# Optimization experiments

Measured on AMD Instinct MI355X. Metric: run time of the kernel, lower is better.

## Reference

```python
import jax, jax.numpy as jnp
import numpy as np

NUM_ITER = 3
SLOT_DIM = 16
INPUT_DIM = 256
HIDDEN_DIM = 128
EPS = 1e-8
LN_EPS = 1e-5  # torch LayerNorm default


def _layernorm(x, w, b):
    mu = jnp.mean(x, axis=-1, keepdims=True)
    var = jnp.mean((x - mu) ** 2, axis=-1, keepdims=True)
    return (x - mu) * jax.lax.rsqrt(var + LN_EPS) * w + b


def setup_inputs() -> dict:
    key = jax.random.key(0)
    ks = jax.random.split(key, 12)
    B, N, K = 32, 4096, 8
    D, S, H = INPUT_DIM, SLOT_DIM, HIDDEN_DIM
    inputs = jax.random.normal(ks[0], (B, N, D), dtype=jnp.float32)
    init_slots = jax.random.normal(ks[1], (B, K, S), dtype=jnp.float32)
    return {
        "inputs": inputs,
        "init_slots": init_slots,
        "ln_in_w": jnp.ones((D,), jnp.float32),
        "ln_in_b": jnp.zeros((D,), jnp.float32),
        "ln_s_w": jnp.ones((S,), jnp.float32),
        "ln_s_b": jnp.zeros((S,), jnp.float32),
        "ln_m_w": jnp.ones((S,), jnp.float32),
        "ln_m_b": jnp.zeros((S,), jnp.float32),
        "wq": jax.random.normal(ks[2], (S, S), jnp.float32) * (S ** -0.5),
        "wk": jax.random.normal(ks[3], (S, D), jnp.float32) * (D ** -0.5),
        "wv": jax.random.normal(ks[4], (S, D), jnp.float32) * (D ** -0.5),
        "w_ih": jax.random.normal(ks[5], (3 * S, S), jnp.float32) * (S ** -0.5),
        "w_hh": jax.random.normal(ks[6], (3 * S, S), jnp.float32) * (S ** -0.5),
        "b_ih": jnp.zeros((3 * S,), jnp.float32),
        "b_hh": jnp.zeros((3 * S,), jnp.float32),
        "mlp_w1": jax.random.normal(ks[7], (H, S), jnp.float32) * (S ** -0.5),
        "mlp_b1": jnp.zeros((H,), jnp.float32),
        "mlp_w2": jax.random.normal(ks[8], (S, H), jnp.float32) * (H ** -0.5),
        "mlp_b2": jnp.zeros((S,), jnp.float32),
    }


def _gru_cell(x, h, w_ih, w_hh, b_ih, b_hh):
    # torch GRUCell: gates ordered [r, z, n]
    gi = x @ w_ih.T + b_ih            # [BK, 3S]
    gh = h @ w_hh.T + b_hh
    i_r, i_z, i_n = jnp.split(gi, 3, axis=-1)
    h_r, h_z, h_n = jnp.split(gh, 3, axis=-1)
    r = jax.nn.sigmoid(i_r + h_r)
    z = jax.nn.sigmoid(i_z + h_z)
    n = jnp.tanh(i_n + r * h_n)
    return (1.0 - z) * n + z * h


def reference(inputs, init_slots, ln_in_w, ln_in_b, ln_s_w, ln_s_b, ln_m_w, ln_m_b,
              wq, wk, wv, w_ih, w_hh, b_ih, b_hh, mlp_w1, mlp_b1, mlp_w2, mlp_b2):
    B, N, _ = inputs.shape
    K = init_slots.shape[1]
    scale = SLOT_DIM ** -0.5

    x = _layernorm(inputs, ln_in_w, ln_in_b)
    k = jnp.einsum('bnd,sd->bns', x, wk)   # [B,N,S]
    v = jnp.einsum('bnd,sd->bns', x, wv)

    slots = init_slots
    attn = None
    for _ in range(NUM_ITER):
        slots_prev = slots
        q = jnp.einsum('bks,ts->bkt', _layernorm(slots, ln_s_w, ln_s_b), wq)
        logits = jnp.einsum('bks,bns->bkn', q, k) * scale       # [B,K,N]
        attn = jax.nn.softmax(logits, axis=1) + EPS              # softmax over SLOTS
        attn = attn / jnp.sum(attn, axis=-1, keepdims=True)
        updates = jnp.einsum('bkn,bns->bks', attn, v)            # [B,K,S]
        h = _gru_cell(updates.reshape(B * K, -1), slots_prev.reshape(B * K, -1),
                      w_ih, w_hh, b_ih, b_hh).reshape(B, K, -1)
        y = _layernorm(h, ln_m_w, ln_m_b)
        mlp = jax.nn.relu(y @ mlp_w1.T + mlp_b1) @ mlp_w2.T + mlp_b2
        slots = h + mlp
    return slots, attn
```

## Files before the change

kernel.cpp:

```cpp
#include <hip/hip_runtime.h>
#include <cstddef>


typedef unsigned short ushort_t;
typedef __attribute__((ext_vector_type(8))) short short8;
typedef __attribute__((ext_vector_type(4))) float f32x4;

__device__ __forceinline__ float sigmoid_f(float x){ return 1.f/(1.f+__expf(-x)); }
__device__ __forceinline__ float tanh_f(float x){ return 1.f - 2.f/(__expf(2.f*x)+1.f); }

__device__ __forceinline__ ushort_t f2bf(float x){
  unsigned u = __float_as_uint(x);
  return (ushort_t)((u + 0x7FFFu + ((u>>16)&1u)) >> 16);
}
__device__ __forceinline__ float bf2f(ushort_t b){
  return __uint_as_float(((unsigned)b) << 16);
}
__device__ __forceinline__ void split_bf(float v, short& hi, short& lo){
  unsigned u = __float_as_uint(v);
  hi = (short)(u >> 16);
  float hf = __uint_as_float(u & 0xFFFF0000u);
  lo = (short)(__float_as_uint(v - hf) >> 16);
}

__device__ __forceinline__ void load16_to_lds(const float* g, float* l) {
  __builtin_amdgcn_global_load_lds(
      (const __attribute__((address_space(1))) unsigned int*)g,
      (__attribute__((address_space(3))) unsigned int*)l,
      16, 0, 0);
}

__global__ __launch_bounds__(256) void k_prep(
    const float* __restrict__ lnw, const float* __restrict__ lnb,
    const float* __restrict__ wk, const float* __restrict__ wv,
    const float* __restrict__ init_slots,
    const float* __restrict__ ln_s_w, const float* __restrict__ ln_s_b,
    const float* __restrict__ wq,
    ushort_t* __restrict__ Wh, ushort_t* __restrict__ Wl,
    float* __restrict__ mt,
    float* __restrict__ qbuf, float* __restrict__ upd, float* __restrict__ Abuf,
    float* __restrict__ slots_out)
{
  int t = threadIdx.x;
  int i = blockIdx.x*256 + t;
  {
    int s = i >> 8, d = i & 255;
    float w = (s < 16) ? wk[s*256+d] : wv[(s-16)*256+d];
    float w0 = lnw[d]*w;
    ushort_t hb = f2bf(w0);
    ushort_t lb = f2bf(w0 - bf2f(hb));
    Wh[i] = hb; Wl[i] = lb;
  }
  if (blockIdx.x != 0) return;
  {
    int s = t >> 3, j = t & 7;
    float m = 0.f, tv = 0.f;
    for (int d = j; d < 256; d += 8) {
      float w = (s < 16) ? wk[s*256+d] : wv[(s-16)*256+d];
      float w0 = lnw[d]*w;
      ushort_t hb = f2bf(w0);
      float hf = bf2f(hb);
      float lf = bf2f(f2bf(w0 - hf));
      m  += hf + lf;
      tv  = fmaf(lnb[d], w, tv);
    }
    m += __shfl_xor(m,1);  m += __shfl_xor(m,2);  m += __shfl_xor(m,4);
    tv += __shfl_xor(tv,1); tv += __shfl_xor(tv,2); tv += __shfl_xor(tv,4);
    if (j == 0) { mt[s] = m; mt[32+s] = tv; }
  }
  #pragma unroll
  for (int j2 = 0; j2 < 16; ++j2) {
    slots_out[t*16+j2] = init_slots[t*16+j2];
    upd[t*16+j2] = 0.f;
  }
  Abuf[t] = 0.f;
  float sl[16];
  #pragma unroll
  for (int j2 = 0; j2 < 16; ++j2) sl[j2] = init_slots[t*16+j2];
  float mu = 0.f;
  #pragma unroll
  for (int j2 = 0; j2 < 16; ++j2) mu += sl[j2];
  mu *= (1.f/16.f);
  float var = 0.f;
  #pragma unroll
  for (int j2 = 0; j2 < 16; ++j2) { float d = sl[j2]-mu; var = fmaf(d,d,var); }
  var *= (1.f/16.f);
  float rstd = rsqrtf(var + 1e-5f);
  float y[16];
  #pragma unroll
  for (int j2 = 0; j2 < 16; ++j2) y[j2] = (sl[j2]-mu)*rstd*ln_s_w[j2] + ln_s_b[j2];
  #pragma unroll
  for (int tq = 0; tq < 16; ++tq) {
    float q = 0.f;
    #pragma unroll
    for (int s2 = 0; s2 < 16; ++s2) q = fmaf(y[s2], wq[tq*16+s2], q);
    qbuf[t*16+tq] = q;
  }
}

__global__ __launch_bounds__(256, 4) void k_proj(
    const float* __restrict__ x, const ushort_t* __restrict__ Wh,
    const ushort_t* __restrict__ Wl, const float* __restrict__ mt,
    float* __restrict__ kout, float* __restrict__ vout)
{
  __shared__ float xs[2][64*64];
  int t = threadIdx.x;
  int lane = t & 63;
  int p = __builtin_amdgcn_readfirstlane(t >> 6);
  int m = lane & 15, quad = lane >> 4;
  int r0 = blockIdx.x*64;
  const float* xbase = x + (size_t)r0*256;

  int sr = lane >> 4;
  int slot = lane & 15;
  int row_st0 = p*16 + sr;
  int cb0 = (slot - row_st0) & 15;

  const ushort_t* whk = Wh + (size_t)m*256 + quad*8;
  const ushort_t* whv = whk + 16*256;
  const ushort_t* wlk = Wl + (size_t)m*256 + quad*8;
  const ushort_t* wlv = wlk + 16*256;

  #define ISSUE_CHUNK(c_, buf_)                                              \
    _Pragma("unroll")                                                        \
    for (int i = 0; i < 4; ++i) {                                            \
      int row = row_st0 + i*4;                                               \
      int cb  = (cb0 - i*4) & 15;                                            \
      load16_to_lds(xbase + (size_t)row*256 + (c_)*64 + cb*4,                \
                    &xs[buf_][(p*16 + i*4)*64]);                             \
    }

  f32x4 acck = {0.f,0.f,0.f,0.f}, accv = {0.f,0.f,0.f,0.f};
  float sum = 0.f, sumsq = 0.f;

  ISSUE_CHUNK(0, 0)
  __syncthreads();

  int rowA = p*16 + m;
  #pragma unroll 1
  for (int c = 0; c < 4; ++c) {
    if (c < 3) { ISSUE_CHUNK(c+1, (c+1)&1) }
    const float* xb = xs[c&1];
    #pragma unroll
    for (int ks = 0; ks < 2; ++ks) {
      int kk = c*2 + ks;
      short8 bh_k = *(const short8*)(whk + kk*32);
      short8 bh_v = *(const short8*)(whv + kk*32);
      short8 bl_k = *(const short8*)(wlk + kk*32);
      short8 bl_v = *(const short8*)(wlv + kk*32);
      int cbA = ks*8 + quad*2;
      float4 f0 = *(const float4*)&xb[rowA*64 + (((cbA  ) + m) & 15)*4];
      float4 f1 = *(const float4*)&xb[rowA*64 + (((cbA+1) + m) & 15)*4];
      float xv[8] = {f0.x,f0.y,f0.z,f0.w, f1.x,f1.y,f1.z,f1.w};
      short8 ah, al;
      #pragma unroll
      for (int j = 0; j < 8; ++j) {
        float v = xv[j];
        sum += v; sumsq = fmaf(v, v, sumsq);
        short h_, l_;
        split_bf(v, h_, l_);
        ah[j] = h_; al[j] = l_;
      }
      acck = __builtin_amdgcn_mfma_f32_16x16x32_bf16(ah, bh_k, acck, 0, 0, 0);
      accv = __builtin_amdgcn_mfma_f32_16x16x32_bf16(ah, bh_v, accv, 0, 0, 0);
      acck = __builtin_amdgcn_mfma_f32_16x16x32_bf16(al, bh_k, acck, 0, 0, 0);
      accv = __builtin_amdgcn_mfma_f32_16x16x32_bf16(al, bh_v, accv, 0, 0, 0);
      acck = __builtin_amdgcn_mfma_f32_16x16x32_bf16(ah, bl_k, acck, 0, 0, 0);
      accv = __builtin_amdgcn_mfma_f32_16x16x32_bf16(ah, bl_v, accv, 0, 0, 0);
    }
    __syncthreads();
  }
  #undef ISSUE_CHUNK

  sum   += __shfl_xor(sum, 16);  sum   += __shfl_xor(sum, 32);
  sumsq += __shfl_xor(sumsq, 16); sumsq += __shfl_xor(sumsq, 32);

  float mtk  = mt[m],    mtv  = mt[16+m];
  float mtkb = mt[32+m], mtvb = mt[48+m];
  #pragma unroll
  for (int r = 0; r < 4; ++r) {
    int row = quad*4 + r;
    float s_ = __shfl(sum,   row);
    float q_ = __shfl(sumsq, row);
    float mu = s_*(1.f/256.f);
    float var = q_*(1.f/256.f) - mu*mu;
    float rstd = rsqrtf(var + 1e-5f);
    float ok = fmaf(rstd, acck[r] - mu*mtk, mtkb);
    float ov = fmaf(rstd, accv[r] - mu*mtv, mtvb);
    size_t grow = (size_t)(r0 + p*16 + row)*16 + m;
    kout[grow] = ok;
    vout[grow] = ov;
  }
}

__global__ __launch_bounds__(256) void k_attn(
    const float* __restrict__ kproj, const float* __restrict__ vproj,
    const float* __restrict__ qbuf,
    float* __restrict__ upd, float* __restrict__ Abuf,
    float* __restrict__ attn_out, int write_attn)
{
  __shared__ ushort_t vt[32*264];
  __shared__ ushort_t pt[32*264];
  __shared__ float qs[128];
  __shared__ float apart[4][8];
  int b = blockIdx.x >> 4;
  int n0 = (blockIdx.x & 15) * 256;
  int t = threadIdx.x;
  int w = t >> 6, lane = t & 63;

  if (t < 128) qs[t] = qbuf[b*128 + t];

  const float* kr = kproj + ((size_t)(b*4096 + n0 + t))*16;
  const float* vr = vproj + ((size_t)(b*4096 + n0 + t))*16;
  float kv[16], vv[16];
  #pragma unroll
  for (int j = 0; j < 16; j += 4) {
    float4 f = *(const float4*)(kr+j);
    kv[j]=f.x; kv[j+1]=f.y; kv[j+2]=f.z; kv[j+3]=f.w;
    float4 g = *(const float4*)(vr+j);
    vv[j]=g.x; vv[j+1]=g.y; vv[j+2]=g.z; vv[j+3]=g.w;
  }
  #pragma unroll
  for (int s = 0; s < 16; ++s) {
    short h_, l_;
    split_bf(vv[s], h_, l_);
    vt[s*264 + t] = (ushort_t)h_;
    vt[(16+s)*264 + t] = (ushort_t)l_;
  }
  __syncthreads();

  float p8[8];
  {
    float lg[8];
    #pragma unroll
    for (int kk = 0; kk < 8; ++kk) {
      float a = 0.f;
      #pragma unroll
      for (int s = 0; s < 16; ++s) a = fmaf(qs[kk*16+s], kv[s], a);
      lg[kk] = a*0.25f;
    }
    float mx = lg[0];
    #pragma unroll
    for (int kk = 1; kk < 8; ++kk) mx = fmaxf(mx, lg[kk]);
    float se = 0.f;
    #pragma unroll
    for (int kk = 0; kk < 8; ++kk) { lg[kk] = __expf(lg[kk]-mx); se += lg[kk]; }
    float inv = 1.f/se;
    #pragma unroll
    for (int kk = 0; kk < 8; ++kk) {
      float pv = fmaf(lg[kk], inv, 1e-8f);
      p8[kk] = pv;
      if (write_attn) attn_out[((size_t)(b*8+kk))*4096 + n0 + t] = pv;
    }
  }
  #pragma unroll
  for (int kk = 0; kk < 8; ++kk) {
    float r = p8[kk];
    r += __shfl_xor(r, 1);  r += __shfl_xor(r, 2);  r += __shfl_xor(r, 4);
    r += __shfl_xor(r, 8);  r += __shfl_xor(r, 16); r += __shfl_xor(r, 32);
    if (lane == 0) apart[w][kk] = r;
  }
  #pragma unroll
  for (int kk = 0; kk < 8; ++kk) {
    short h_, l_;
    split_bf(p8[kk], h_, l_);
    pt[kk*264 + t] = (ushort_t)h_;
    pt[(16+kk)*264 + t] = (ushort_t)l_;
  }
  __syncthreads();

  if (t < 8)
    atomicAdd(Abuf + b*8 + t,
              apart[0][t] + apart[1][t] + apart[2][t] + apart[3][t]);

  if (w == 0) {
    int m = lane & 15, quad = lane >> 4;
    const short8 z8 = {0,0,0,0,0,0,0,0};
    f32x4 acc = {0.f,0.f,0.f,0.f};
    #pragma unroll
    for (int c = 0; c < 8; ++c) {
      int k0 = c*32 + quad*8;
      short8 ah = (m < 8) ? *(const short8*)&pt[m*264 + k0]      : z8;
      short8 al = (m < 8) ? *(const short8*)&pt[(16+m)*264 + k0] : z8;
      short8 bh = *(const short8*)&vt[m*264 + k0];
      short8 bl = *(const short8*)&vt[(16+m)*264 + k0];
      acc = __builtin_amdgcn_mfma_f32_16x16x32_bf16(ah, bh, acc, 0, 0, 0);
      acc = __builtin_amdgcn_mfma_f32_16x16x32_bf16(al, bh, acc, 0, 0, 0);
      acc = __builtin_amdgcn_mfma_f32_16x16x32_bf16(ah, bl, acc, 0, 0, 0);
    }
    int s = lane & 15;
    #pragma unroll
    for (int r = 0; r < 4; ++r) {
      int kk = quad*4 + r;
      if (kk < 8) atomicAdd(upd + (b*8+kk)*16 + s, acc[r]);
    }
  }
}

__global__ __launch_bounds__(256) void k_gru(
    float* __restrict__ upd, float* __restrict__ Abuf,
    float* __restrict__ slots, float* __restrict__ qbuf,
    const float* __restrict__ w_ih, const float* __restrict__ w_hh,
    const float* __restrict__ b_ih, const float* __restrict__ b_hh,
    const float* __restrict__ mlp_w1, const float* __restrict__ mlp_b1,
    const float* __restrict__ mlp_w2, const float* __restrict__ mlp_b2,
    const float* __restrict__ ln_m_w, const float* __restrict__ ln_m_b,
    const float* __restrict__ ln_s_w, const float* __restrict__ ln_s_b,
    const float* __restrict__ wq, int prep_next)
{
  __shared__ float s_wih[48*17], s_whh[48*17];
  __shared__ float s_bih[48], s_bhh[48];
  __shared__ float s_w1[128*17], s_b1[128];
  __shared__ float s_w2[16*129], s_b2[16];
  __shared__ float s_lnmw[16], s_lnmb[16], s_lnsw[16], s_lnsb[16];
  __shared__ float s_wq[16*17];
  int t = threadIdx.x;
  for (int i = t; i < 768; i += 256) {
    int g = i >> 4, j = i & 15;
    s_wih[g*17+j] = w_ih[i];
    s_whh[g*17+j] = w_hh[i];
  }
  for (int i = t; i < 2048; i += 256) {
    int r = i >> 4, c = i & 15;
    s_w1[r*17+c] = mlp_w1[i];
    int r2 = i >> 7, c2 = i & 127;
    s_w2[r2*129+c2] = mlp_w2[i];
  }
  if (t < 48) { s_bih[t] = b_ih[t]; s_bhh[t] = b_hh[t]; }
  if (t < 128) s_b1[t] = mlp_b1[t];
  if (t < 16) {
    s_b2[t] = mlp_b2[t];
    s_lnmw[t] = ln_m_w[t]; s_lnmb[t] = ln_m_b[t];
    s_lnsw[t] = ln_s_w[t]; s_lnsb[t] = ln_s_b[t];
  }
  for (int i = t; i < 256; i += 256) {
    int r = i >> 4, c = i & 15;
    s_wq[r*17+c] = wq[i];
  }
  __syncthreads();

  int bk = blockIdx.x*16 + (t >> 4);
  int s = t & 15;
  int laneBase = (t & 63) & ~15;

  float inv = 1.f / Abuf[bk];
  float u[16], h[16];
  #pragma unroll
  for (int j = 0; j < 16; ++j) {
    u[j] = upd[bk*16+j] * inv;
    h[j] = slots[bk*16+j];
  }
  float hs = slots[bk*16+s];

  float gir = s_bih[s],  giz = s_bih[16+s], gin = s_bih[32+s];
  float ghr = s_bhh[s],  ghz = s_bhh[16+s], ghn = s_bhh[32+s];
  #pragma unroll
  for (int j = 0; j < 16; ++j) {
    gir = fmaf(u[j], s_wih[s*17+j], gir);
    giz = fmaf(u[j], s_wih[(16+s)*17+j], giz);
    gin = fmaf(u[j], s_wih[(32+s)*17+j], gin);
    ghr = fmaf(h[j], s_whh[s*17+j], ghr);
    ghz = fmaf(h[j], s_whh[(16+s)*17+j], ghz);
    ghn = fmaf(h[j], s_whh[(32+s)*17+j], ghn);
  }
  float rr = sigmoid_f(gir + ghr);
  float zz = sigmoid_f(giz + ghz);
  float nn = tanh_f(gin + rr*ghn);
  float hn = (1.f-zz)*nn + zz*hs;

  float ssum = hn;
  #pragma unroll
  for (int mm = 1; mm < 16; mm <<= 1) ssum += __shfl_xor(ssum, mm);
  float mu = ssum*(1.f/16.f);
  float dv = hn - mu;
  float vs = dv*dv;
  #pragma unroll
  for (int mm = 1; mm < 16; mm <<= 1) vs += __shfl_xor(vs, mm);
  float rstd = rsqrtf(vs*(1.f/16.f) + 1e-5f);
  float y = dv*rstd*s_lnmw[s] + s_lnmb[s];

  float yv[16];
  #pragma unroll
  for (int j = 0; j < 16; ++j) yv[j] = __shfl(y, laneBase + j);

  float h1[8];
  #pragma unroll
  for (int i = 0; i < 8; ++i) {
    int jj = i*16 + s;
    float a = s_b1[jj];
    #pragma unroll
    for (int q = 0; q < 16; ++q) a = fmaf(yv[q], s_w1[jj*17+q], a);
    h1[i] = fmaxf(a, 0.f);
  }
  float o = s_b2[s];
  #pragma unroll
  for (int i = 0; i < 8; ++i) {
    #pragma unroll
    for (int sp = 0; sp < 16; ++sp) {
      float hv = __shfl(h1[i], laneBase + sp);
      o = fmaf(hv, s_w2[s*129 + i*16 + sp], o);
    }
  }
  float slot_new = hn + o;
  slots[bk*16+s] = slot_new;

  if (prep_next) {
    float ss = slot_new;
    #pragma unroll
    for (int mm = 1; mm < 16; mm <<= 1) ss += __shfl_xor(ss, mm);
    float mu2 = ss*(1.f/16.f);
    float d2 = slot_new - mu2;
    float v2 = d2*d2;
    #pragma unroll
    for (int mm = 1; mm < 16; mm <<= 1) v2 += __shfl_xor(v2, mm);
    float rstd2 = rsqrtf(v2*(1.f/16.f) + 1e-5f);
    float y2 = d2*rstd2*s_lnsw[s] + s_lnsb[s];
    float qv = 0.f;
    #pragma unroll
    for (int sp = 0; sp < 16; ++sp)
      qv = fmaf(__shfl(y2, laneBase+sp), s_wq[s*17+sp], qv);
    qbuf[bk*16+s] = qv;
    upd[bk*16+s] = 0.f;
    if (s == 0) Abuf[bk] = 0.f;
  }
}

__global__ __launch_bounds__(256) void k_scale(float* __restrict__ attn,
                                               const float* __restrict__ Abuf)
{
  int bk = blockIdx.x;
  float inv = 1.f / Abuf[bk];
  float4* p = (float4*)(attn + (size_t)bk*4096);
  #pragma unroll 4
  for (int i = threadIdx.x; i < 1024; i += 256) {
    float4 v = p[i];
    v.x *= inv; v.y *= inv; v.z *= inv; v.w *= inv;
    p[i] = v;
  }
}

extern "C" void kernel_launch(void* const* d_in, const int* in_sizes, int n_in,
                              void* d_out, int out_size, void* d_ws, size_t ws_size,
                              hipStream_t stream)
{
  const float* inputs     = (const float*)d_in[0];
  const float* init_slots = (const float*)d_in[1];
  const float* ln_in_w    = (const float*)d_in[2];
  const float* ln_in_b    = (const float*)d_in[3];
  const float* ln_s_w     = (const float*)d_in[4];
  const float* ln_s_b     = (const float*)d_in[5];
  const float* ln_m_w     = (const float*)d_in[6];
  const float* ln_m_b     = (const float*)d_in[7];
  const float* wq         = (const float*)d_in[8];
  const float* wk         = (const float*)d_in[9];
  const float* wv         = (const float*)d_in[10];
  const float* w_ih       = (const float*)d_in[11];
  const float* w_hh       = (const float*)d_in[12];
  const float* b_ih       = (const float*)d_in[13];
  const float* b_hh       = (const float*)d_in[14];
  const float* mlp_w1     = (const float*)d_in[15];
  const float* mlp_b1     = (const float*)d_in[16];
  const float* mlp_w2     = (const float*)d_in[17];
  const float* mlp_b2     = (const float*)d_in[18];

  float* ws    = (float*)d_ws;
  ushort_t* Wh = (ushort_t*)ws;
  ushort_t* Wl = (ushort_t*)(ws + 4096);
  float* mt    = ws + 8192;
  float* qbuf  = ws + 8320;
  float* upd   = ws + 12416;
  float* Abuf  = ws + 16512;
  float* kproj = ws + 16768;
  float* vproj = kproj + 2097152;

  float* out   = (float*)d_out;
  float* slots = out;
  float* attn  = out + 4096;

  k_prep<<<32, 256, 0, stream>>>(ln_in_w, ln_in_b, wk, wv, init_slots,
                                 ln_s_w, ln_s_b, wq,
                                 Wh, Wl, mt, qbuf, upd, Abuf, slots);
  k_proj<<<2048, 256, 0, stream>>>(inputs, Wh, Wl, mt, kproj, vproj);
  for (int it = 0; it < 3; ++it) {
    int last = (it == 2);
    k_attn<<<512, 256, 0, stream>>>(kproj, vproj, qbuf, upd, Abuf, attn, last);
    k_gru<<<16, 256, 0, stream>>>(upd, Abuf, slots, qbuf,
                                  w_ih, w_hh, b_ih, b_hh,
                                  mlp_w1, mlp_b1, mlp_w2, mlp_b2,
                                  ln_m_w, ln_m_b, ln_s_w, ln_s_b,
                                  wq, last ? 0 : 1);
  }
  k_scale<<<256, 256, 0, stream>>>(attn, Abuf);
}
```

Baseline: 298.0 us.

## Load whole input tile into LDS in k_proj and fuse final GRU with attn scaling

k_proj drops its double-buffered 64-column chunk pipeline and instead loads the entire 64x256 input tile into LDS up front (64 KB), then runs all 8 k-steps without intermediate barriers. The launch-bounds occupancy hint is removed, since the larger LDS footprint lowers the number of resident blocks anyway. The last GRU launch is merged with the attention rescale kernel into one k_final kernel, which saves one launch. The risk is less latency hiding in k_proj because load and compute no longer overlap and fewer blocks fit per CU.

Result: no change. 299.4 us (+0.5%).

```diff
diff --git a/kernel.cpp b/kernel.cpp
--- a/kernel.cpp
+++ b/kernel.cpp
@@ -98,12 +98,12 @@
   }
 }
 
-__global__ __launch_bounds__(256, 4) void k_proj(
+__global__ __launch_bounds__(256) void k_proj(
     const float* __restrict__ x, const ushort_t* __restrict__ Wh,
     const ushort_t* __restrict__ Wl, const float* __restrict__ mt,
     float* __restrict__ kout, float* __restrict__ vout)
 {
-  __shared__ float xs[2][64*64];
+  __shared__ float xs[64*256];
   int t = threadIdx.x;
   int lane = t & 63;
   int p = __builtin_amdgcn_readfirstlane(t >> 6);
@@ -111,66 +111,54 @@
   int r0 = blockIdx.x*64;
   const float* xbase = x + (size_t)r0*256;
 
-  int sr = lane >> 4;
-  int slot = lane & 15;
-  int row_st0 = p*16 + sr;
-  int cb0 = (slot - row_st0) & 15;
-
   const ushort_t* whk = Wh + (size_t)m*256 + quad*8;
   const ushort_t* whv = whk + 16*256;
   const ushort_t* wlk = Wl + (size_t)m*256 + quad*8;
   const ushort_t* wlv = wlk + 16*256;
 
-  #define ISSUE_CHUNK(c_, buf_)                                              \
-    _Pragma("unroll")                                                        \
-    for (int i = 0; i < 4; ++i) {                                            \
-      int row = row_st0 + i*4;                                               \
-      int cb  = (cb0 - i*4) & 15;                                            \
-      load16_to_lds(xbase + (size_t)row*256 + (c_)*64 + cb*4,                \
-                    &xs[buf_][(p*16 + i*4)*64]);                             \
-    }
+  {
+    int c = lane >> 4, slot = lane & 15;
+    #pragma unroll
+    for (int i = 0; i < 16; ++i) {
+      int row = p*16 + i;
+      int cb = (slot - row) & 15;
+      load16_to_lds(xbase + (size_t)row*256 + c*64 + cb*4, &xs[row*256]);
+    }
+  }
+  __syncthreads();
 
   f32x4 acck = {0.f,0.f,0.f,0.f}, accv = {0.f,0.f,0.f,0.f};
   float sum = 0.f, sumsq = 0.f;
-
-  ISSUE_CHUNK(0, 0)
-  __syncthreads();
-
   int rowA = p*16 + m;
-  #pragma unroll 1
-  for (int c = 0; c < 4; ++c) {
-    if (c < 3) { ISSUE_CHUNK(c+1, (c+1)&1) }
-    const float* xb = xs[c&1];
-    #pragma unroll
-    for (int ks = 0; ks < 2; ++ks) {
-      int kk = c*2 + ks;
-      short8 bh_k = *(const short8*)(whk + kk*32);
-      short8 bh_v = *(const short8*)(whv + kk*32);
-      short8 bl_k = *(const short8*)(wlk + kk*32);
-      short8 bl_v = *(const short8*)(wlv + kk*32);
-      int cbA = ks*8 + quad*2;
-      float4 f0 = *(const float4*)&xb[rowA*64 + (((cbA  ) + m) & 15)*4];
-      float4 f1 = *(const float4*)&xb[rowA*64 + (((cbA+1) + m) & 15)*4];
-      float xv[8] = {f0.x,f0.y,f0.z,f0.w, f1.x,f1.y,f1.z,f1.w};
-      short8 ah, al;
-      #pragma unroll
-      for (int j = 0; j < 8; ++j) {
-        float v = xv[j];
-        sum += v; sumsq = fmaf(v, v, sumsq);
-        short h_, l_;
-        split_bf(v, h_, l_);
-        ah[j] = h_; al[j] = l_;
-      }
-      acck = __builtin_amdgcn_mfma_f32_16x16x32_bf16(ah, bh_k, acck, 0, 0, 0);
-      accv = __builtin_amdgcn_mfma_f32_16x16x32_bf16(ah, bh_v, accv, 0, 0, 0);
-      acck = __builtin_amdgcn_mfma_f32_16x16x32_bf16(al, bh_k, acck, 0, 0, 0);
-      accv = __builtin_amdgcn_mfma_f32_16x16x32_bf16(al, bh_v, accv, 0, 0, 0);
-      acck = __builtin_amdgcn_mfma_f32_16x16x32_bf16(ah, bl_k, acck, 0, 0, 0);
-      accv = __builtin_amdgcn_mfma_f32_16x16x32_bf16(ah, bl_v, accv, 0, 0, 0);
-    }
-    __syncthreads();
-  }
-  #undef ISSUE_CHUNK
+  const float* xrow = &xs[rowA*256];
+
+  #pragma unroll
+  for (int kk = 0; kk < 8; ++kk) {
+    int c = kk >> 1, ks = kk & 1;
+    short8 bh_k = *(const short8*)(whk + kk*32);
+    short8 bh_v = *(const short8*)(whv + kk*32);
+    short8 bl_k = *(const short8*)(wlk + kk*32);
+    short8 bl_v = *(const short8*)(wlv + kk*32);
+    int cbA = ks*8 + quad*2;
+    float4 f0 = *(const float4*)&xrow[c*64 + (((cbA  ) + m) & 15)*4];
+    float4 f1 = *(const float4*)&xrow[c*64 + (((cbA+1) + m) & 15)*4];
+    float xv[8] = {f0.x,f0.y,f0.z,f0.w, f1.x,f1.y,f1.z,f1.w};
+    short8 ah, al;
+    #pragma unroll
+    for (int j = 0; j < 8; ++j) {
+      float v = xv[j];
+      sum += v; sumsq = fmaf(v, v, sumsq);
+      short h_, l_;
+      split_bf(v, h_, l_);
+      ah[j] = h_; al[j] = l_;
+    }
+    acck = __builtin_amdgcn_mfma_f32_16x16x32_bf16(ah, bh_k, acck, 0, 0, 0);
+    accv = __builtin_amdgcn_mfma_f32_16x16x32_bf16(ah, bh_v, accv, 0, 0, 0);
+    acck = __builtin_amdgcn_mfma_f32_16x16x32_bf16(al, bh_k, acck, 0, 0, 0);
+    accv = __builtin_amdgcn_mfma_f32_16x16x32_bf16(al, bh_v, accv, 0, 0, 0);
+    acck = __builtin_amdgcn_mfma_f32_16x16x32_bf16(ah, bl_k, acck, 0, 0, 0);
+    accv = __builtin_amdgcn_mfma_f32_16x16x32_bf16(ah, bl_v, accv, 0, 0, 0);
+  }
 
   sum   += __shfl_xor(sum, 16);  sum   += __shfl_xor(sum, 32);
   sumsq += __shfl_xor(sumsq, 16); sumsq += __shfl_xor(sumsq, 32);
@@ -297,6 +285,132 @@
   }
 }
 
+__device__ __forceinline__ void gru_body(
+    int bk, int s, int laneBase, int prep_next,
+    float* upd, float* Abuf, float* slots, float* qbuf,
+    const float* s_wih, const float* s_whh,
+    const float* s_bih, const float* s_bhh,
+    const float* s_w1, const float* s_b1,
+    const float* s_w2, const float* s_b2,
+    const float* s_lnmw, const float* s_lnmb,
+    const float* s_lnsw, const float* s_lnsb, const float* s_wq)
+{
+  float inv = 1.f / Abuf[bk];
+  float u[16], h[16];
+  #pragma unroll
+  for (int j = 0; j < 16; ++j) {
+    u[j] = upd[bk*16+j] * inv;
+    h[j] = slots[bk*16+j];
+  }
+  float hs = slots[bk*16+s];
+
+  float gir = s_bih[s],  giz = s_bih[16+s], gin = s_bih[32+s];
+  float ghr = s_bhh[s],  ghz = s_bhh[16+s], ghn = s_bhh[32+s];
+  #pragma unroll
+  for (int j = 0; j < 16; ++j) {
+    gir = fmaf(u[j], s_wih[s*17+j], gir);
+    giz = fmaf(u[j], s_wih[(16+s)*17+j], giz);
+    gin = fmaf(u[j], s_wih[(32+s)*17+j], gin);
+    ghr = fmaf(h[j], s_whh[s*17+j], ghr);
+    ghz = fmaf(h[j], s_whh[(16+s)*17+j], ghz);
+    ghn = fmaf(h[j], s_whh[(32+s)*17+j], ghn);
+  }
+  float rr = sigmoid_f(gir + ghr);
+  float zz = sigmoid_f(giz + ghz);
+  float nn = tanh_f(gin + rr*ghn);
+  float hn = (1.f-zz)*nn + zz*hs;
+
+  float ssum = hn;
+  #pragma unroll
+  for (int mm = 1; mm < 16; mm <<= 1) ssum += __shfl_xor(ssum, mm);
+  float mu = ssum*(1.f/16.f);
+  float dv = hn - mu;
+  float vs = dv*dv;
+  #pragma unroll
+  for (int mm = 1; mm < 16; mm <<= 1) vs += __shfl_xor(vs, mm);
+  float rstd = rsqrtf(vs*(1.f/16.f) + 1e-5f);
+  float y = dv*rstd*s_lnmw[s] + s_lnmb[s];
+
+  float yv[16];
+  #pragma unroll
+  for (int j = 0; j < 16; ++j) yv[j] = __shfl(y, laneBase + j);
+
+  float h1[8];
+  #pragma unroll
+  for (int i = 0; i < 8; ++i) {
+    int jj = i*16 + s;
+    float a = s_b1[jj];
+    #pragma unroll
+    for (int q = 0; q < 16; ++q) a = fmaf(yv[q], s_w1[jj*17+q], a);
+    h1[i] = fmaxf(a, 0.f);
+  }
+  float o = s_b2[s];
+  #pragma unroll
+  for (int i = 0; i < 8; ++i) {
+    #pragma unroll
+    for (int sp = 0; sp < 16; ++sp) {
+      float hv = __shfl(h1[i], laneBase + sp);
+      o = fmaf(hv, s_w2[s*129 + i*16 + sp], o);
+    }
+  }
+  float slot_new = hn + o;
+  slots[bk*16+s] = slot_new;
+
+  if (prep_next) {
+    float ss = slot_new;
+    #pragma unroll
+    for (int mm = 1; mm < 16; mm <<= 1) ss += __shfl_xor(ss, mm);
+    float mu2 = ss*(1.f/16.f);
+    float d2 = slot_new - mu2;
+    float v2 = d2*d2;
+    #pragma unroll
+    for (int mm = 1; mm < 16; mm <<= 1) v2 += __shfl_xor(v2, mm);
+    float rstd2 = rsqrtf(v2*(1.f/16.f) + 1e-5f);
+    float y2 = d2*rstd2*s_lnsw[s] + s_lnsb[s];
+    float qv = 0.f;
+    #pragma unroll
+    for (int sp = 0; sp < 16; ++sp)
+      qv = fmaf(__shfl(y2, laneBase+sp), s_wq[s*17+sp], qv);
+    qbuf[bk*16+s] = qv;
+    upd[bk*16+s] = 0.f;
+    if (s == 0) Abuf[bk] = 0.f;
+  }
+}
+
+#define GRU_STAGE_LDS()                                                      \
+  __shared__ float s_wih[48*17], s_whh[48*17];                               \
+  __shared__ float s_bih[48], s_bhh[48];                                     \
+  __shared__ float s_w1[128*17], s_b1[128];                                  \
+  __shared__ float s_w2[16*129], s_b2[16];                                   \
+  __shared__ float s_lnmw[16], s_lnmb[16], s_lnsw[16], s_lnsb[16];           \
+  __shared__ float s_wq[16*17];                                              \
+  {                                                                          \
+    int t_ = threadIdx.x;                                                    \
+    for (int i = t_; i < 768; i += 256) {                                    \
+      int g = i >> 4, j = i & 15;                                            \
+      s_wih[g*17+j] = w_ih[i];                                               \
+      s_whh[g*17+j] = w_hh[i];                                               \
+    }                                                                        \
+    for (int i = t_; i < 2048; i += 256) {                                   \
+      int r = i >> 4, c = i & 15;                                            \
+      s_w1[r*17+c] = mlp_w1[i];                                              \
+      int r2 = i >> 7, c2 = i & 127;                                         \
+      s_w2[r2*129+c2] = mlp_w2[i];                                           \
+    }                                                                        \
+    if (t_ < 48) { s_bih[t_] = b_ih[t_]; s_bhh[t_] = b_hh[t_]; }             \
+    if (t_ < 128) s_b1[t_] = mlp_b1[t_];                                     \
+    if (t_ < 16) {                                                           \
+      s_b2[t_] = mlp_b2[t_];                                                 \
+      s_lnmw[t_] = ln_m_w[t_]; s_lnmb[t_] = ln_m_b[t_];                      \
+      s_lnsw[t_] = ln_s_w[t_]; s_lnsb[t_] = ln_s_b[t_];                      \
+    }                                                                        \
+    for (int i = t_; i < 256; i += 256) {                                    \
+      int r = i >> 4, c = i & 15;                                            \
+      s_wq[r*17+c] = wq[i];                                                  \
+    }                                                                        \
+  }                                                                          \
+  __syncthreads();
+
 __global__ __launch_bounds__(256) void k_gru(
     float* __restrict__ upd, float* __restrict__ Abuf,
     float* __restrict__ slots, float* __restrict__ qbuf,
@@ -306,137 +420,50 @@
     const float* __restrict__ mlp_w2, const float* __restrict__ mlp_b2,
     const float* __restrict__ ln_m_w, const float* __restrict__ ln_m_b,
     const float* __restrict__ ln_s_w, const float* __restrict__ ln_s_b,
-    const float* __restrict__ wq, int prep_next)
-{
-  __shared__ float s_wih[48*17], s_whh[48*17];
-  __shared__ float s_bih[48], s_bhh[48];
-  __shared__ float s_w1[128*17], s_b1[128];
-  __shared__ float s_w2[16*129], s_b2[16];
-  __shared__ float s_lnmw[16], s_lnmb[16], s_lnsw[16], s_lnsb[16];
-  __shared__ float s_wq[16*17];
+    const float* __restrict__ wq)
+{
+  GRU_STAGE_LDS()
   int t = threadIdx.x;
-  for (int i = t; i < 768; i += 256) {
-    int g = i >> 4, j = i & 15;
-    s_wih[g*17+j] = w_ih[i];
-    s_whh[g*17+j] = w_hh[i];
-  }
-  for (int i = t; i < 2048; i += 256) {
-    int r = i >> 4, c = i & 15;
-    s_w1[r*17+c] = mlp_w1[i];
-    int r2 = i >> 7, c2 = i & 127;
-    s_w2[r2*129+c2] = mlp_w2[i];
-  }
-  if (t < 48) { s_bih[t] = b_ih[t]; s_bhh[t] = b_hh[t]; }
-  if (t < 128) s_b1[t] = mlp_b1[t];
-  if (t < 16) {
-    s_b2[t] = mlp_b2[t];
-    s_lnmw[t] = ln_m_w[t]; s_lnmb[t] = ln_m_b[t];
-    s_lnsw[t] = ln_s_w[t]; s_lnsb[t] = ln_s_b[t];
-  }
-  for (int i = t; i < 256; i += 256) {
-    int r = i >> 4, c = i & 15;
-    s_wq[r*17+c] = wq[i];
-  }
-  __syncthreads();
-
   int bk = blockIdx.x*16 + (t >> 4);
   int s = t & 15;
   int laneBase = (t & 63) & ~15;
-
-  float inv = 1.f / Abuf[bk];
-  float u[16], h[16];
-  #pragma unroll
-  for (int j = 0; j < 16; ++j) {
-    u[j] = upd[bk*16+j] * inv;
-    h[j] = slots[bk*16+j];
-  }
-  float hs = slots[bk*16+s];
-
-  float gir = s_bih[s],  giz = s_bih[16+s], gin = s_bih[32+s];
-  float ghr = s_bhh[s],  ghz = s_bhh[16+s], ghn = s_bhh[32+s];
-  #pragma unroll
-  for (int j = 0; j < 16; ++j) {
-    gir = fmaf(u[j], s_wih[s*17+j], gir);
-    giz = fmaf(u[j], s_wih[(16+s)*17+j], giz);
-    gin = fmaf(u[j], s_wih[(32+s)*17+j], gin);
-    ghr = fmaf(h[j], s_whh[s*17+j], ghr);
-    ghz = fmaf(h[j], s_whh[(16+s)*17+j], ghz);
-    ghn = fmaf(h[j], s_whh[(32+s)*17+j], ghn);
-  }
-  float rr = sigmoid_f(gir + ghr);
-  float zz = sigmoid_f(giz + ghz);
-  float nn = tanh_f(gin + rr*ghn);
-  float hn = (1.f-zz)*nn + zz*hs;
-
-  float ssum = hn;
-  #pragma unroll
-  for (int mm = 1; mm < 16; mm <<= 1) ssum += __shfl_xor(ssum, mm);
-  float mu = ssum*(1.f/16.f);
-  float dv = hn - mu;
-  float vs = dv*dv;
-  #pragma unroll
-  for (int mm = 1; mm < 16; mm <<= 1) vs += __shfl_xor(vs, mm);
-  float rstd = rsqrtf(vs*(1.f/16.f) + 1e-5f);
-  float y = dv*rstd*s_lnmw[s] + s_lnmb[s];
-
-  float yv[16];
-  #pragma unroll
-  for (int j = 0; j < 16; ++j) yv[j] = __shfl(y, laneBase + j);
-
-  float h1[8];
-  #pragma unroll
-  for (int i = 0; i < 8; ++i) {
-    int jj = i*16 + s;
-    float a = s_b1[jj];
-    #pragma unroll
-    for (int q = 0; q < 16; ++q) a = fmaf(yv[q], s_w1[jj*17+q], a);
-    h1[i] = fmaxf(a, 0.f);
-  }
-  float o = s_b2[s];
-  #pragma unroll
-  for (int i = 0; i < 8; ++i) {
-    #pragma unroll
-    for (int sp = 0; sp < 16; ++sp) {
-      float hv = __shfl(h1[i], laneBase + sp);
-      o = fmaf(hv, s_w2[s*129 + i*16 + sp], o);
-    }
-  }
-  float slot_new = hn + o;
-  slots[bk*16+s] = slot_new;
-
-  if (prep_next) {
-    float ss = slot_new;
-    #pragma unroll
-    for (int mm = 1; mm < 16; mm <<= 1) ss += __shfl_xor(ss, mm);
-    float mu2 = ss*(1.f/16.f);
-    float d2 = slot_new - mu2;
-    float v2 = d2*d2;
-    #pragma unroll
-    for (int mm = 1; mm < 16; mm <<= 1) v2 += __shfl_xor(v2, mm);
-    float rstd2 = rsqrtf(v2*(1.f/16.f) + 1e-5f);
-    float y2 = d2*rstd2*s_lnsw[s] + s_lnsb[s];
-    float qv = 0.f;
-    #pragma unroll
-    for (int sp = 0; sp < 16; ++sp)
-      qv = fmaf(__shfl(y2, laneBase+sp), s_wq[s*17+sp], qv);
-    qbuf[bk*16+s] = qv;
-    upd[bk*16+s] = 0.f;
-    if (s == 0) Abuf[bk] = 0.f;
-  }
-}
-
-__global__ __launch_bounds__(256) void k_scale(float* __restrict__ attn,
-                                               const float* __restrict__ Abuf)
-{
-  int bk = blockIdx.x;
-  float inv = 1.f / Abuf[bk];
-  float4* p = (float4*)(attn + (size_t)bk*4096);
-  #pragma unroll 4
-  for (int i = threadIdx.x; i < 1024; i += 256) {
-    float4 v = p[i];
-    v.x *= inv; v.y *= inv; v.z *= inv; v.w *= inv;
-    p[i] = v;
-  }
+  gru_body(bk, s, laneBase, 1, upd, Abuf, slots, qbuf,
+           s_wih, s_whh, s_bih, s_bhh, s_w1, s_b1, s_w2, s_b2,
+           s_lnmw, s_lnmb, s_lnsw, s_lnsb, s_wq);
+}
+
+__global__ __launch_bounds__(256) void k_final(
+    float* __restrict__ upd, float* __restrict__ Abuf,
+    float* __restrict__ slots, float* __restrict__ qbuf,
+    float* __restrict__ attn,
+    const float* __restrict__ w_ih, const float* __restrict__ w_hh,
+    const float* __restrict__ b_ih, const float* __restrict__ b_hh,
+    const float* __restrict__ mlp_w1, const float* __restrict__ mlp_b1,
+    const float* __restrict__ mlp_w2, const float* __restrict__ mlp_b2,
+    const float* __restrict__ ln_m_w, const float* __restrict__ ln_m_b,
+    const float* __restrict__ ln_s_w, const float* __restrict__ ln_s_b,
+    const float* __restrict__ wq)
+{
+  int t = threadIdx.x;
+  {
+    int bk = blockIdx.x;
+    float inv = 1.f / Abuf[bk];
+    float4* p = (float4*)(attn + (size_t)bk*4096);
+    #pragma unroll 4
+    for (int i = t; i < 1024; i += 256) {
+      float4 v = p[i];
+      v.x *= inv; v.y *= inv; v.z *= inv; v.w *= inv;
+      p[i] = v;
+    }
+  }
+  if (blockIdx.x >= 16) return;
+  GRU_STAGE_LDS()
+  int bk = blockIdx.x*16 + (t >> 4);
+  int s = t & 15;
+  int laneBase = (t & 63) & ~15;
+  gru_body(bk, s, laneBase, 0, upd, Abuf, slots, qbuf,
+           s_wih, s_whh, s_bih, s_bhh, s_w1, s_b1, s_w2, s_b2,
+           s_lnmw, s_lnmb, s_lnsw, s_lnsb, s_wq);
 }
 
 extern "C" void kernel_launch(void* const* d_in, const int* in_sizes, int n_in,
@@ -484,11 +511,14 @@
   for (int it = 0; it < 3; ++it) {
     int last = (it == 2);
     k_attn<<<512, 256, 0, stream>>>(kproj, vproj, qbuf, upd, Abuf, attn, last);
-    k_gru<<<16, 256, 0, stream>>>(upd, Abuf, slots, qbuf,
-                                  w_ih, w_hh, b_ih, b_hh,
-                                  mlp_w1, mlp_b1, mlp_w2, mlp_b2,
-                                  ln_m_w, ln_m_b, ln_s_w, ln_s_b,
-                                  wq, last ? 0 : 1);
-  }
-  k_scale<<<256, 256, 0, stream>>>(attn, Abuf);
-}
+    if (!last)
+      k_gru<<<16, 256, 0, stream>>>(upd, Abuf, slots, qbuf,
+                                    w_ih, w_hh, b_ih, b_hh,
+                                    mlp_w1, mlp_b1, mlp_w2, mlp_b2,
+                                    ln_m_w, ln_m_b, ln_s_w, ln_s_b, wq);
+  }
+  k_final<<<256, 256, 0, stream>>>(upd, Abuf, slots, qbuf, attn,
+                                   w_ih, w_hh, b_ih, b_hh,
+                                   mlp_w1, mlp_b1, mlp_w2, mlp_b2,
+                                   ln_m_w, ln_m_b, ln_s_w, ln_s_b, wq);
+}
```
